# Optimization experiments

Measured on AMD Instinct MI355X. Metric: run time of the kernel, lower is better.

## Reference

```python
import jax, jax.numpy as jnp
import numpy as np
from jax import lax

B, T, D = 4, 2048, 2048
H, K, V = 16, 128, 128
CONV_K = 4
EPS_G = 1e-6
LN_EPS = 1e-5


def _dconv_causal(x, w, b):
    # x: (B,T,C); w: (C,1,Kk) depthwise. torch pads both sides Kk-1 then slices [:T],
    # which equals a causal left-pad of Kk-1.
    y = lax.conv_general_dilated(
        jnp.transpose(x, (0, 2, 1)), w, (1,),
        [(w.shape[-1] - 1, 0)],
        dimension_numbers=('NCH', 'OIH', 'NCH'),
        feature_group_count=w.shape[0])
    return jnp.transpose(y + b[None, :, None], (0, 2, 1))


def _kda_scan(q, k, v, g, beta, scale):
    # q,k: (B,H,T,K); v: (B,H,T,V); g: (B,H,T,K) log-decay (channel-wise); beta: (B,H,T)
    # Gated delta rule: S_t = Diag(exp(g_t)) S_{t-1} + beta_t k_t (v_t - k_t^T Diag(exp(g_t)) S_{t-1})
    S0 = jnp.zeros(q.shape[:2] + (q.shape[-1], v.shape[-1]), q.dtype)

    def step(S, inp):
        qt, kt, vt, gt, bt = inp
        S = S * jnp.exp(gt)[..., :, None]                     # per-key-channel decay
        err = vt - jnp.einsum('bhk,bhkv->bhv', kt, S)         # delta correction
        S = S + bt[..., None, None] * kt[..., None] * err[..., None, :]
        o = scale * jnp.einsum('bhk,bhkv->bhv', qt, S)
        return S, o

    xs = tuple(jnp.moveaxis(t_, 2, 0) for t_ in (q, k, v, g)) + (jnp.moveaxis(beta, 2, 0),)
    _, o = lax.scan(step, S0, xs)
    return jnp.moveaxis(o, 0, 2)                              # (B,H,T,V)


def setup_inputs() -> dict:
    key = jax.random.key(0)
    ks = jax.random.split(key, 16)
    s = 0.02
    return {
        'x':   jax.random.normal(ks[0], (B, T, D), jnp.float32),
        'Wq':  jax.random.normal(ks[1], (H * K, D), jnp.float32) * s,
        'Wk':  jax.random.normal(ks[2], (H * K, D), jnp.float32) * s,
        'Wv':  jax.random.normal(ks[3], (H * V, D), jnp.float32) * s,
        'Wa':  jax.random.normal(ks[4], (H * V, D), jnp.float32) * s,
        'ba':  jax.random.normal(ks[5], (H * V,), jnp.float32) * s,
        'Wb':  jax.random.normal(ks[6], (H, D), jnp.float32) * s,
        'bb':  jax.random.normal(ks[7], (H,), jnp.float32) * s,
        'Wg':  jax.random.normal(ks[8], (H * V, D), jnp.float32) * s,
        'Wo':  jax.random.normal(ks[9], (D, H * V), jnp.float32) * s,
        'cqw': jax.random.normal(ks[10], (H * K, 1, CONV_K), jnp.float32) * 0.2,
        'cqb': jnp.zeros((H * K,), jnp.float32),
        'ckw': jax.random.normal(ks[11], (H * K, 1, CONV_K), jnp.float32) * 0.2,
        'ckb': jnp.zeros((H * K,), jnp.float32),
        'cvw': jax.random.normal(ks[12], (H * V, 1, CONV_K), jnp.float32) * 0.2,
        'cvb': jnp.zeros((H * V,), jnp.float32),
        'ln_w': jnp.ones((V,), jnp.float32),
        'ln_b': jnp.zeros((V,), jnp.float32),
    }


def reference(x, Wq, Wk, Wv, Wa, ba, Wb, bb, Wg, Wo,
              cqw, cqb, ckw, ckb, cvw, cvb, ln_w, ln_b):
    b, t, _ = x.shape
    scale = K ** -0.5
    q = jax.nn.silu(_dconv_causal(x @ Wq.T, cqw, cqb))
    k = jax.nn.silu(_dconv_causal(x @ Wk.T, ckw, ckb))
    v = jax.nn.silu(_dconv_causal(x @ Wv.T, cvw, cvb))
    q = q.reshape(b, t, H, K).transpose(0, 2, 1, 3)           # (B,H,T,K)
    k = k.reshape(b, t, H, K).transpose(0, 2, 1, 3)
    v = v.reshape(b, t, H, V).transpose(0, 2, 1, 3)
    a = jax.nn.sigmoid(x @ Wa.T + ba).reshape(b, t, H, V).transpose(0, 2, 1, 3)
    g = jnp.log(jnp.maximum(a, EPS_G))                        # log-space channel gate
    beta = jax.nn.sigmoid(x @ Wb.T + bb).transpose(0, 2, 1)   # (B,H,T)
    o = _kda_scan(q, k, v, g, beta, scale).transpose(0, 2, 1, 3)  # (B,T,H,V)
    mu = o.mean(-1, keepdims=True)
    var = ((o - mu) ** 2).mean(-1, keepdims=True)
    o = (o - mu) * lax.rsqrt(var + LN_EPS) * ln_w + ln_b      # per-head LayerNorm
    gate = jax.nn.sigmoid(x @ Wg.T).reshape(b, t, H, V)
    return ((o * gate).reshape(b, t, H * V)) @ Wo.T
```

## Files before the change

kernel.cpp:

```cpp
#include <hip/hip_runtime.h>
#include <cstdint>
#include <cstddef>

#define B_ 4
#define T_ 2048
#define D_ 2048
#define H_ 16

typedef __bf16 bf16x8 __attribute__((ext_vector_type(8)));
typedef float  f32x4  __attribute__((ext_vector_type(4)));
typedef unsigned short u16;
typedef u16 u16x8 __attribute__((ext_vector_type(8)));

__device__ __forceinline__ u16 f2bf(float f) {
    union { float f; unsigned u; } v; v.f = f;
    unsigned r = v.u + 0x7FFFu + ((v.u >> 16) & 1u);
    return (u16)(r >> 16);
}
__device__ __forceinline__ float bf2f(u16 h) {
    union { unsigned u; float f; } v; v.u = ((unsigned)h) << 16;
    return v.f;
}
__device__ __forceinline__ float sigmoidf_(float x) {
    return 1.f / (1.f + __expf(-x));
}
__device__ __forceinline__ void async_load16(const void* g, void* l) {
    __builtin_amdgcn_global_load_lds(
        (const __attribute__((address_space(1))) void*)g,
        (__attribute__((address_space(3))) void*)l,
        16, 0, 0);
}

__device__ __forceinline__ float row_allreduce16(float x) {
    int v;
    v = __builtin_amdgcn_update_dpp(0, __builtin_bit_cast(int, x), 0xB1, 0xF, 0xF, true);
    x += __builtin_bit_cast(float, v);
    v = __builtin_amdgcn_update_dpp(0, __builtin_bit_cast(int, x), 0x4E, 0xF, 0xF, true);
    x += __builtin_bit_cast(float, v);
    v = __builtin_amdgcn_update_dpp(0, __builtin_bit_cast(int, x), 0x140, 0xF, 0xF, true);
    x += __builtin_bit_cast(float, v);
    v = __builtin_amdgcn_update_dpp(0, __builtin_bit_cast(int, x), 0x141, 0xF, 0xF, true);
    x += __builtin_bit_cast(float, v);
    return x;
}

__global__ void cvt_bf16_k(const float* __restrict__ s, u16* __restrict__ d, int n) {
    int i = blockIdx.x * 256 + threadIdx.x;
    if (i < n) d[i] = f2bf(s[i]);
}

__global__ void pad_wb_k(const float* __restrict__ Wb, u16* __restrict__ d) {
    int i = blockIdx.x * 256 + threadIdx.x;
    d[i] = (i < 32768) ? f2bf(Wb[i]) : (u16)0;
}

__device__ __forceinline__ void store_c(float* p, float v) { *p = v; }
__device__ __forceinline__ void store_c(u16* p, float v) { *p = f2bf(v); }

template <typename OutT, int PERM>
__global__ __launch_bounds__(256) void gemm_bt(const u16* __restrict__ A,
                                               const u16* __restrict__ Bm,
                                               OutT* __restrict__ C, int K, int ldc) {
    __shared__ __align__(16) u16 smA[128 * 64];
    __shared__ __align__(16) u16 smB[128 * 64];
    const int tid  = threadIdx.x;
    const int lane = tid & 63;
    const int w    = tid >> 6;
    const int wm   = (w >> 1) * 64;
    const int wn   = (w & 1) * 64;
    const int bm   = blockIdx.x, bn = blockIdx.y;

    f32x4 acc[4][4];
#pragma unroll
    for (int i = 0; i < 4; ++i)
#pragma unroll
        for (int j = 0; j < 4; ++j) acc[i][j] = (f32x4){0.f, 0.f, 0.f, 0.f};

    const int rr = tid >> 3;
    const int cc = (tid & 7) * 8;
    const u16* Ag = A + (size_t)(bm * 128) * K;
    const u16* Bg = Bm + (size_t)(bn * 128) * K;

    for (int k0 = 0; k0 < K; k0 += 64) {
#pragma unroll
        for (int it = 0; it < 4; ++it) {
            async_load16(Ag + (size_t)(it * 32 + rr) * K + (k0 + cc), &smA[(it * 256 + tid) * 8]);
            async_load16(Bg + (size_t)(it * 32 + rr) * K + (k0 + cc), &smB[(it * 256 + tid) * 8]);
        }
        __syncthreads();
#pragma unroll
        for (int kk = 0; kk < 64; kk += 32) {
            bf16x8 af[4], bfr[4];
            const int qoff = kk + ((lane >> 4) * 8);
#pragma unroll
            for (int mi = 0; mi < 4; ++mi)
                af[mi] = *(const bf16x8*)&smA[(wm + mi * 16 + (lane & 15)) * 64 + qoff];
#pragma unroll
            for (int ni = 0; ni < 4; ++ni)
                bfr[ni] = *(const bf16x8*)&smB[(wn + ni * 16 + (lane & 15)) * 64 + qoff];
#pragma unroll
            for (int mi = 0; mi < 4; ++mi)
#pragma unroll
                for (int ni = 0; ni < 4; ++ni)
                    acc[mi][ni] = __builtin_amdgcn_mfma_f32_16x16x32_bf16(af[mi], bfr[ni], acc[mi][ni], 0, 0, 0);
        }
        __syncthreads();
    }

#pragma unroll
    for (int mi = 0; mi < 4; ++mi) {
        const int row0 = bm * 128 + wm + mi * 16 + ((lane >> 4) * 4);
#pragma unroll
        for (int ni = 0; ni < 4; ++ni) {
            int colg = bn * 128 + wn + ni * 16 + (lane & 15);
            if (PERM) colg = (colg & ~127) | (((colg & 15) << 3) | ((colg >> 4) & 7));
#pragma unroll
            for (int rg = 0; rg < 4; ++rg)
                store_c(&C[(size_t)(row0 + rg) * ldc + colg], acc[mi][ni][rg]);
        }
    }
}

template <int TRANSPOSE>
__global__ void conv_silu_k(const u16* __restrict__ pre,
                            const float* __restrict__ w, const float* __restrict__ bias,
                            u16* __restrict__ outp) {
    int idx = blockIdx.x * 256 + threadIdx.x;
    int c = idx & 2047;
    int t = (idx >> 11) & (T_ - 1);
    int b = idx >> 22;
    const u16* base = pre + (size_t)(b * T_ + t) * 2048 + c;
    float acc = bias[c];
#pragma unroll
    for (int j = 0; j < 4; ++j) {
        int tt = t - 3 + j;
        if (tt >= 0) {
            float xv = bf2f(base[(ptrdiff_t)(j - 3) * 2048]);
            acc = fmaf(xv, w[c * 4 + j], acc);
        }
    }
    float y = acc * sigmoidf_(acc);
    int h = c >> 7, cl = c & 127;
    int p = TRANSPOSE ? ((cl & 15) * 8 + (cl >> 4)) : cl;
    outp[((size_t)(b * H_ + h) * T_ + t) * 128 + p] = f2bf(y);
}

#define TB 8
__global__ __launch_bounds__(256) void kda_scan_k(const u16* __restrict__ qg,
                                                  const u16* __restrict__ kg,
                                                  const u16* __restrict__ vg,
                                                  const u16* __restrict__ ag,
                                                  const u16* __restrict__ bpg,
                                                  const float* __restrict__ bav,
                                                  const float* __restrict__ bbv,
                                                  u16* __restrict__ og) {
    const int blk = blockIdx.x;
    const int bh  = blk >> 3;
    const int vch = blk & 7;
    const int tid = threadIdx.x;
    const int col = tid >> 4;
    const int sl  = tid & 15;
    const int b = bh >> 4, h = bh & 15;

    __shared__ __align__(16) u16   sq[2][TB][128];
    __shared__ __align__(16) u16   sk[2][TB][128];
    __shared__ __align__(16) float sdA[2][TB][64];
    __shared__ __align__(16) float sdB[2][TB][64];
    __shared__ float sv[2][TB][16];
    __shared__ float sb_[2][TB];

    const u16* qb  = qg + (size_t)bh * T_ * 128;
    const u16* kb  = kg + (size_t)bh * T_ * 128;
    const u16* vb  = vg + (size_t)bh * T_ * 128 + vch * 16;
    const u16* ab  = ag + (size_t)b * T_ * 2048 + h * 128;
    const u16* bpb = bpg + (size_t)b * T_ * 128 + h;
    u16* op = og + (size_t)b * T_ * 2048 + h * 128 + vch * 16 + col;

    const int ur = tid >> 5;
    const int c4 = (tid & 31) * 4;
    const int chb = c4 >> 3;
    const int jb  = c4 & 7;
    const float rba0 = bav[h * 128 + (jb + 0) * 16 + chb];
    const float rba1 = bav[h * 128 + (jb + 1) * 16 + chb];
    const float rba2 = bav[h * 128 + (jb + 2) * 16 + chb];
    const float rba3 = bav[h * 128 + (jb + 3) * 16 + chb];
    const float bbh = bbv[h];
    float* dst_d = (c4 & 4) ? &sdB[0][0][0] : &sdA[0][0][0];
    const int doff = ur * 64 + chb * 4;
    const int dstride = TB * 64;

    float S[8];
#pragma unroll
    for (int j = 0; j < 8; ++j) S[j] = 0.f;

    ushort4 rq, rk, ra;
    float rv = 0.f, rbet = 0.f;
    rq = *(const ushort4*)(qb + tid * 4);
    rk = *(const ushort4*)(kb + tid * 4);
    ra = *(const ushort4*)(ab + (size_t)ur * 2048 + c4);
    if (tid < 128) rv = bf2f(vb[(size_t)(tid >> 4) * 128 + (tid & 15)]);
    if (tid < TB) rbet = bf2f(bpb[(size_t)tid * 128]);

    const float scale = 0.08838834764831845f;
    const int NM = T_ / TB;
    for (int m = 0; m < NM; ++m) {
        const int pb = m & 1;
        float4 fd = {fmaxf(sigmoidf_(bf2f(ra.x) + rba0), 1e-6f),
                     fmaxf(sigmoidf_(bf2f(ra.y) + rba1), 1e-6f),
                     fmaxf(sigmoidf_(bf2f(ra.z) + rba2), 1e-6f),
                     fmaxf(sigmoidf_(bf2f(ra.w) + rba3), 1e-6f)};
        *(ushort4*)(&sq[pb][0][0] + tid * 4) = rq;
        *(ushort4*)(&sk[pb][0][0] + tid * 4) = rk;
        *(float4*)(dst_d + pb * dstride + doff) = fd;
        if (tid < 128) sv[pb][tid >> 4][tid & 15] = rv;
        if (tid < TB) sb_[pb][tid] = sigmoidf_(rbet + bbh);
        __syncthreads();
        if (m + 1 < NM) {
            size_t t0n = (size_t)(m + 1) * TB;
            rq = *(const ushort4*)(qb + t0n * 128 + tid * 4);
            rk = *(const ushort4*)(kb + t0n * 128 + tid * 4);
            ra = *(const ushort4*)(ab + (t0n + ur) * 2048 + c4);
            if (tid < 128) rv = bf2f(vb[(t0n + (tid >> 4)) * 128 + (tid & 15)]);
            if (tid < TB) rbet = bf2f(bpb[(t0n + tid) * 128]);
        }
#pragma unroll
        for (int u = 0; u < TB; ++u) {
            u16x8 q8 = *(const u16x8*)&sq[pb][u][sl * 8];
            u16x8 k8 = *(const u16x8*)&sk[pb][u][sl * 8];
            float4 dA = *(const float4*)&sdA[pb][u][sl * 4];
            float4 dB = *(const float4*)&sdB[pb][u][sl * 4];
            float kf[8], qf[8], dv[8];
#pragma unroll
            for (int j = 0; j < 8; ++j) { kf[j] = bf2f(k8[j]); qf[j] = bf2f(q8[j]); }
            dv[0] = dA.x; dv[1] = dA.y; dv[2] = dA.z; dv[3] = dA.w;
            dv[4] = dB.x; dv[5] = dB.y; dv[6] = dB.z; dv[7] = dB.w;
            float e0 = 0.f, e1 = 0.f;
#pragma unroll
            for (int j = 0; j < 8; j += 2) {
                S[j]     *= dv[j];     e0 = fmaf(kf[j],     S[j],     e0);
                S[j + 1] *= dv[j + 1]; e1 = fmaf(kf[j + 1], S[j + 1], e1);
            }
            float errp = row_allreduce16(e0 + e1);
            float uu = sb_[pb][u] * (sv[pb][u][col] - errp);
            float o0 = 0.f, o1 = 0.f;
#pragma unroll
            for (int j = 0; j < 8; j += 2) {
                S[j]     = fmaf(kf[j],     uu, S[j]);     o0 = fmaf(qf[j],     S[j],     o0);
                S[j + 1] = fmaf(kf[j + 1], uu, S[j + 1]); o1 = fmaf(qf[j + 1], S[j + 1], o1);
            }
            float outv = row_allreduce16(o0 + o1);
            if (sl == 0) op[(size_t)(m * TB + u) * 2048] = f2bf(scale * outv);
        }
        __syncthreads();
    }
}

__global__ __launch_bounds__(256) void ln_gate_k(const u16* __restrict__ o,
                                                 const u16* __restrict__ gpre,
                                                 const float* __restrict__ lnw,
                                                 const float* __restrict__ lnb,
                                                 u16* __restrict__ act) {
    int inst = blockIdx.x * 4 + (threadIdx.x >> 6);
    int lane = threadIdx.x & 63;
    int bt = inst >> 4, h = inst & 15;
    const u16* opr = o + (size_t)bt * 2048 + h * 128;
    ushort2 xr = *(const ushort2*)(opr + lane * 2);
    float x0 = bf2f(xr.x), x1 = bf2f(xr.y);
    float s  = x0 + x1;
    float ss = x0 * x0 + x1 * x1;
#pragma unroll
    for (int msk = 1; msk < 64; msk <<= 1) {
        s  += __shfl_xor(s, msk);
        ss += __shfl_xor(ss, msk);
    }
    float mu   = s * (1.f / 128.f);
    float var  = ss * (1.f / 128.f) - mu * mu;
    float rstd = rsqrtf(var + 1e-5f);
    const u16* gp = gpre + (size_t)bt * 2048 + h * 128 + lane * 2;
    u16* ap = act + (size_t)bt * 2048 + h * 128 + lane * 2;
#pragma unroll
    for (int e = 0; e < 2; ++e) {
        int v = lane * 2 + e;
        float xx = (e == 0) ? x0 : x1;
        float y = (xx - mu) * rstd * lnw[v] + lnb[v];
        float gate = sigmoidf_(bf2f(gp[e]));
        ap[e] = f2bf(y * gate);
    }
}

extern "C" void kernel_launch(void* const* d_in, const int* in_sizes, int n_in,
                              void* d_out, int out_size, void* d_ws, size_t ws_size,
                              hipStream_t stream) {
    (void)in_sizes; (void)n_in; (void)out_size; (void)ws_size;
    const float* x   = (const float*)d_in[0];
    const float* Wq  = (const float*)d_in[1];
    const float* Wk  = (const float*)d_in[2];
    const float* Wv  = (const float*)d_in[3];
    const float* Wa  = (const float*)d_in[4];
    const float* ba  = (const float*)d_in[5];
    const float* Wb  = (const float*)d_in[6];
    const float* bbv = (const float*)d_in[7];
    const float* Wg  = (const float*)d_in[8];
    const float* Wo  = (const float*)d_in[9];
    const float* cqw = (const float*)d_in[10];
    const float* cqb = (const float*)d_in[11];
    const float* ckw = (const float*)d_in[12];
    const float* ckb = (const float*)d_in[13];
    const float* cvw = (const float*)d_in[14];
    const float* cvb = (const float*)d_in[15];
    const float* lnw = (const float*)d_in[16];
    const float* lnb = (const float*)d_in[17];
    float* out = (float*)d_out;

    char* p = (char*)d_ws;
    size_t off = 0;
    auto take = [&](size_t bytes) -> char* {
        char* r = p + off;
        off += (bytes + 255) & ~(size_t)255;
        return r;
    };
    u16* Wslot = (u16*)take((size_t)4194304 * 2);
    u16* qpre  = (u16*)take((size_t)16777216 * 2);
    u16* kpre  = (u16*)take((size_t)16777216 * 2);
    u16* vpre  = (u16*)take((size_t)16777216 * 2);
    u16* apre  = (u16*)take((size_t)16777216 * 2);
    u16* bpre  = (u16*)take((size_t)1048576 * 2);

    u16* xb  = (u16*)d_out;
    u16* qsc = (u16*)d_out + 16777216;
    u16* ksc  = qpre;
    u16* vsc  = kpre;
    u16* ob   = vpre;
    u16* gpre = qpre;
    u16* act  = kpre;

    cvt_bf16_k<<<65536, 256, 0, stream>>>(x, xb, 16777216);

    cvt_bf16_k<<<16384, 256, 0, stream>>>(Wq, Wslot, 4194304);
    gemm_bt<u16, 0><<<dim3(64, 16), 256, 0, stream>>>(xb, Wslot, qpre, 2048, 2048);
    cvt_bf16_k<<<16384, 256, 0, stream>>>(Wk, Wslot, 4194304);
    gemm_bt<u16, 0><<<dim3(64, 16), 256, 0, stream>>>(xb, Wslot, kpre, 2048, 2048);
    cvt_bf16_k<<<16384, 256, 0, stream>>>(Wv, Wslot, 4194304);
    gemm_bt<u16, 0><<<dim3(64, 16), 256, 0, stream>>>(xb, Wslot, vpre, 2048, 2048);
    cvt_bf16_k<<<16384, 256, 0, stream>>>(Wa, Wslot, 4194304);
    gemm_bt<u16, 1><<<dim3(64, 16), 256, 0, stream>>>(xb, Wslot, apre, 2048, 2048);
    pad_wb_k<<<1024, 256, 0, stream>>>(Wb, Wslot);
    gemm_bt<u16, 0><<<dim3(64, 1), 256, 0, stream>>>(xb, Wslot, bpre, 2048, 128);

    conv_silu_k<1><<<65536, 256, 0, stream>>>(qpre, cqw, cqb, qsc);
    conv_silu_k<1><<<65536, 256, 0, stream>>>(kpre, ckw, ckb, ksc);
    conv_silu_k<0><<<65536, 256, 0, stream>>>(vpre, cvw, cvb, vsc);

    kda_scan_k<<<512, 256, 0, stream>>>(qsc, ksc, vsc, apre, bpre, ba, bbv, ob);

    cvt_bf16_k<<<16384, 256, 0, stream>>>(Wg, Wslot, 4194304);
    gemm_bt<u16, 0><<<dim3(64, 16), 256, 0, stream>>>(xb, Wslot, gpre, 2048, 2048);

    ln_gate_k<<<32768, 256, 0, stream>>>(ob, gpre, lnw, lnb, act);

    cvt_bf16_k<<<16384, 256, 0, stream>>>(Wo, Wslot, 4194304);
    gemm_bt<float, 0><<<dim3(64, 16), 256, 0, stream>>>(act, Wslot, out, 2048, 2048);
}
```

Before: 1.904 ms.

## Split scan state across 32 lanes per value column with 512-thread blocks

The KDA scan kernel now uses 512 threads per block. Each value column's 128-key state is spread over 32 lanes holding 4 entries each, instead of 16 lanes holding 8, which halves the serial per-step work per thread at the cost of an extra cross-half shuffle in each reduction. Q, K and the decay are converted to fp32 once when staged into shared memory. The step tile grows to 16 timesteps, and the block index is remapped to interleave batch-heads across blocks. The permuted channel layout in the GEMM epilogue and the conv kernel is changed to match the new 4-wide per-lane grouping.

Measured after the change: 1.800 ms. -5.5%, faster.

```diff
diff --git a/kernel.cpp b/kernel.cpp
--- a/kernel.cpp
+++ b/kernel.cpp
@@ -41,6 +41,12 @@
     x += __builtin_bit_cast(float, v);
     v = __builtin_amdgcn_update_dpp(0, __builtin_bit_cast(int, x), 0x141, 0xF, 0xF, true);
     x += __builtin_bit_cast(float, v);
+    return x;
+}
+
+__device__ __forceinline__ float grp32_allreduce(float x) {
+    x = row_allreduce16(x);
+    x += __shfl_xor(x, 32);
     return x;
 }
 
@@ -113,7 +119,10 @@
 #pragma unroll
         for (int ni = 0; ni < 4; ++ni) {
             int colg = bn * 128 + wn + ni * 16 + (lane & 15);
-            if (PERM) colg = (colg & ~127) | (((colg & 15) << 3) | ((colg >> 4) & 7));
+            if (PERM) {
+                int cl = colg & 127;
+                colg = (colg & ~127) | (((cl & 31) << 2) | (cl >> 5));
+            }
 #pragma unroll
             for (int rg = 0; rg < 4; ++rg)
                 store_c(&C[(size_t)(row0 + rg) * ldc + colg], acc[mi][ni][rg]);
@@ -141,115 +150,106 @@
     }
     float y = acc * sigmoidf_(acc);
     int h = c >> 7, cl = c & 127;
-    int p = TRANSPOSE ? ((cl & 15) * 8 + (cl >> 4)) : cl;
+    int p = TRANSPOSE ? (((cl & 31) << 2) | (cl >> 5)) : cl;
     outp[((size_t)(b * H_ + h) * T_ + t) * 128 + p] = f2bf(y);
 }
 
-#define TB 8
-__global__ __launch_bounds__(256) void kda_scan_k(const u16* __restrict__ qg,
-                                                  const u16* __restrict__ kg,
-                                                  const u16* __restrict__ vg,
-                                                  const u16* __restrict__ ag,
-                                                  const u16* __restrict__ bpg,
-                                                  const float* __restrict__ bav,
-                                                  const float* __restrict__ bbv,
-                                                  u16* __restrict__ og) {
+#define TB2 16
+__global__ __launch_bounds__(512, 4) void kda_scan_k(const u16* __restrict__ qg,
+                                                     const u16* __restrict__ kg,
+                                                     const u16* __restrict__ vg,
+                                                     const u16* __restrict__ ag,
+                                                     const u16* __restrict__ bpg,
+                                                     const float* __restrict__ bav,
+                                                     const float* __restrict__ bbv,
+                                                     u16* __restrict__ og) {
     const int blk = blockIdx.x;
-    const int bh  = blk >> 3;
-    const int vch = blk & 7;
+    const int bh  = (blk & 7) * 8 + (blk >> 6);
+    const int vch = (blk >> 3) & 7;
     const int tid = threadIdx.x;
-    const int col = tid >> 4;
-    const int sl  = tid & 15;
+    const int lane = tid & 63;
+    const int w    = tid >> 6;
+    const int colIdx = w * 2 + ((lane >> 4) & 1);
+    const int kidx   = (lane & 15) + ((lane >> 5) << 4);
     const int b = bh >> 4, h = bh & 15;
 
-    __shared__ __align__(16) u16   sq[2][TB][128];
-    __shared__ __align__(16) u16   sk[2][TB][128];
-    __shared__ __align__(16) float sdA[2][TB][64];
-    __shared__ __align__(16) float sdB[2][TB][64];
-    __shared__ float sv[2][TB][16];
-    __shared__ float sb_[2][TB];
+    __shared__ __align__(16) float sq[2][TB2][128];
+    __shared__ __align__(16) float sk[2][TB2][128];
+    __shared__ __align__(16) float sd[2][TB2][128];
+    __shared__ float sv[2][TB2][16];
+    __shared__ float sb_[2][TB2];
 
     const u16* qb  = qg + (size_t)bh * T_ * 128;
     const u16* kb  = kg + (size_t)bh * T_ * 128;
     const u16* vb  = vg + (size_t)bh * T_ * 128 + vch * 16;
     const u16* ab  = ag + (size_t)b * T_ * 2048 + h * 128;
     const u16* bpb = bpg + (size_t)b * T_ * 128 + h;
-    u16* op = og + (size_t)b * T_ * 2048 + h * 128 + vch * 16 + col;
+    u16* op = og + (size_t)b * T_ * 2048 + h * 128 + vch * 16 + colIdx;
 
     const int ur = tid >> 5;
-    const int c4 = (tid & 31) * 4;
-    const int chb = c4 >> 3;
-    const int jb  = c4 & 7;
-    const float rba0 = bav[h * 128 + (jb + 0) * 16 + chb];
-    const float rba1 = bav[h * 128 + (jb + 1) * 16 + chb];
-    const float rba2 = bav[h * 128 + (jb + 2) * 16 + chb];
-    const float rba3 = bav[h * 128 + (jb + 3) * 16 + chb];
+    const int p4 = (tid & 31) * 4;
+    const float rba0 = bav[h * 128 +  0 + (tid & 31)];
+    const float rba1 = bav[h * 128 + 32 + (tid & 31)];
+    const float rba2 = bav[h * 128 + 64 + (tid & 31)];
+    const float rba3 = bav[h * 128 + 96 + (tid & 31)];
     const float bbh = bbv[h];
-    float* dst_d = (c4 & 4) ? &sdB[0][0][0] : &sdA[0][0][0];
-    const int doff = ur * 64 + chb * 4;
-    const int dstride = TB * 64;
-
-    float S[8];
-#pragma unroll
-    for (int j = 0; j < 8; ++j) S[j] = 0.f;
+
+    float S[4];
+#pragma unroll
+    for (int j = 0; j < 4; ++j) S[j] = 0.f;
 
     ushort4 rq, rk, ra;
     float rv = 0.f, rbet = 0.f;
-    rq = *(const ushort4*)(qb + tid * 4);
-    rk = *(const ushort4*)(kb + tid * 4);
-    ra = *(const ushort4*)(ab + (size_t)ur * 2048 + c4);
-    if (tid < 128) rv = bf2f(vb[(size_t)(tid >> 4) * 128 + (tid & 15)]);
-    if (tid < TB) rbet = bf2f(bpb[(size_t)tid * 128]);
+    rq = *(const ushort4*)(qb + (size_t)ur * 128 + p4);
+    rk = *(const ushort4*)(kb + (size_t)ur * 128 + p4);
+    ra = *(const ushort4*)(ab + (size_t)ur * 2048 + p4);
+    if (tid < 256) rv = bf2f(vb[(size_t)(tid >> 4) * 128 + (tid & 15)]);
+    if (tid < TB2) rbet = bf2f(bpb[(size_t)tid * 128]);
 
     const float scale = 0.08838834764831845f;
-    const int NM = T_ / TB;
+    const int NM = T_ / TB2;
     for (int m = 0; m < NM; ++m) {
         const int pb = m & 1;
+        float4 fq = {bf2f(rq.x), bf2f(rq.y), bf2f(rq.z), bf2f(rq.w)};
+        float4 fk = {bf2f(rk.x), bf2f(rk.y), bf2f(rk.z), bf2f(rk.w)};
         float4 fd = {fmaxf(sigmoidf_(bf2f(ra.x) + rba0), 1e-6f),
                      fmaxf(sigmoidf_(bf2f(ra.y) + rba1), 1e-6f),
                      fmaxf(sigmoidf_(bf2f(ra.z) + rba2), 1e-6f),
                      fmaxf(sigmoidf_(bf2f(ra.w) + rba3), 1e-6f)};
-        *(ushort4*)(&sq[pb][0][0] + tid * 4) = rq;
-        *(ushort4*)(&sk[pb][0][0] + tid * 4) = rk;
-        *(float4*)(dst_d + pb * dstride + doff) = fd;
-        if (tid < 128) sv[pb][tid >> 4][tid & 15] = rv;
-        if (tid < TB) sb_[pb][tid] = sigmoidf_(rbet + bbh);
+        *(float4*)&sq[pb][ur][p4] = fq;
+        *(float4*)&sk[pb][ur][p4] = fk;
+        *(float4*)&sd[pb][ur][p4] = fd;
+        if (tid < 256) sv[pb][tid >> 4][tid & 15] = rv;
+        if (tid < TB2) sb_[pb][tid] = sigmoidf_(rbet + bbh);
         __syncthreads();
         if (m + 1 < NM) {
-            size_t t0n = (size_t)(m + 1) * TB;
-            rq = *(const ushort4*)(qb + t0n * 128 + tid * 4);
-            rk = *(const ushort4*)(kb + t0n * 128 + tid * 4);
-            ra = *(const ushort4*)(ab + (t0n + ur) * 2048 + c4);
-            if (tid < 128) rv = bf2f(vb[(t0n + (tid >> 4)) * 128 + (tid & 15)]);
-            if (tid < TB) rbet = bf2f(bpb[(t0n + tid) * 128]);
-        }
-#pragma unroll
-        for (int u = 0; u < TB; ++u) {
-            u16x8 q8 = *(const u16x8*)&sq[pb][u][sl * 8];
-            u16x8 k8 = *(const u16x8*)&sk[pb][u][sl * 8];
-            float4 dA = *(const float4*)&sdA[pb][u][sl * 4];
-            float4 dB = *(const float4*)&sdB[pb][u][sl * 4];
-            float kf[8], qf[8], dv[8];
-#pragma unroll
-            for (int j = 0; j < 8; ++j) { kf[j] = bf2f(k8[j]); qf[j] = bf2f(q8[j]); }
-            dv[0] = dA.x; dv[1] = dA.y; dv[2] = dA.z; dv[3] = dA.w;
-            dv[4] = dB.x; dv[5] = dB.y; dv[6] = dB.z; dv[7] = dB.w;
-            float e0 = 0.f, e1 = 0.f;
-#pragma unroll
-            for (int j = 0; j < 8; j += 2) {
-                S[j]     *= dv[j];     e0 = fmaf(kf[j],     S[j],     e0);
-                S[j + 1] *= dv[j + 1]; e1 = fmaf(kf[j + 1], S[j + 1], e1);
-            }
-            float errp = row_allreduce16(e0 + e1);
-            float uu = sb_[pb][u] * (sv[pb][u][col] - errp);
-            float o0 = 0.f, o1 = 0.f;
-#pragma unroll
-            for (int j = 0; j < 8; j += 2) {
-                S[j]     = fmaf(kf[j],     uu, S[j]);     o0 = fmaf(qf[j],     S[j],     o0);
-                S[j + 1] = fmaf(kf[j + 1], uu, S[j + 1]); o1 = fmaf(qf[j + 1], S[j + 1], o1);
-            }
-            float outv = row_allreduce16(o0 + o1);
-            if (sl == 0) op[(size_t)(m * TB + u) * 2048] = f2bf(scale * outv);
+            size_t t0n = (size_t)(m + 1) * TB2;
+            rq = *(const ushort4*)(qb + (t0n + ur) * 128 + p4);
+            rk = *(const ushort4*)(kb + (t0n + ur) * 128 + p4);
+            ra = *(const ushort4*)(ab + (t0n + ur) * 2048 + p4);
+            if (tid < 256) rv = bf2f(vb[(t0n + (tid >> 4)) * 128 + (tid & 15)]);
+            if (tid < TB2) rbet = bf2f(bpb[(t0n + tid) * 128]);
+        }
+#pragma unroll
+        for (int u = 0; u < TB2; ++u) {
+            float4 q4 = *(const float4*)&sq[pb][u][kidx * 4];
+            float4 k4 = *(const float4*)&sk[pb][u][kidx * 4];
+            float4 d4 = *(const float4*)&sd[pb][u][kidx * 4];
+            float e0, e1;
+            S[0] *= d4.x; e0 = k4.x * S[0];
+            S[1] *= d4.y; e1 = k4.y * S[1];
+            S[2] *= d4.z; e0 = fmaf(k4.z, S[2], e0);
+            S[3] *= d4.w; e1 = fmaf(k4.w, S[3], e1);
+            float errp = grp32_allreduce(e0 + e1);
+            float uu = sb_[pb][u] * (sv[pb][u][colIdx] - errp);
+            float o0, o1;
+            S[0] = fmaf(k4.x, uu, S[0]); o0 = q4.x * S[0];
+            S[1] = fmaf(k4.y, uu, S[1]); o1 = q4.y * S[1];
+            S[2] = fmaf(k4.z, uu, S[2]); o0 = fmaf(q4.z, S[2], o0);
+            S[3] = fmaf(k4.w, uu, S[3]); o1 = fmaf(q4.w, S[3], o1);
+            float outv = grp32_allreduce(o0 + o1);
+            if (((lane & 15) | (lane >> 5)) == 0)
+                op[(size_t)(m * TB2 + u) * 2048] = f2bf(scale * outv);
         }
         __syncthreads();
     }
@@ -351,7 +351,7 @@
     conv_silu_k<1><<<65536, 256, 0, stream>>>(kpre, ckw, ckb, ksc);
     conv_silu_k<0><<<65536, 256, 0, stream>>>(vpre, cvw, cvb, vsc);
 
-    kda_scan_k<<<512, 256, 0, stream>>>(qsc, ksc, vsc, apre, bpre, ba, bbv, ob);
+    kda_scan_k<<<512, 512, 0, stream>>>(qsc, ksc, vsc, apre, bpre, ba, bbv, ob);
 
     cvt_bf16_k<<<16384, 256, 0, stream>>>(Wg, Wslot, 4194304);
     gemm_bt<u16, 0><<<dim3(64, 16), 256, 0, stream>>>(xb, Wslot, gpre, 2048, 2048);
```

## Restructure scan to 512-thread blocks with 32 value columns, XCD-aware mapping, vectorize conversion

Applied to the files above, without the earlier changes.

The scan kernel now runs 256 blocks of 512 threads, each covering 32 value columns and 16 timesteps per staging step instead of 16 columns and 8 timesteps. Block indices are remapped so that blocks sharing a (batch, head) land on the same XCD. The goal is to halve redundant q/k/decay loads across blocks and halve the number of barriers per sequence, at the cost of fewer blocks in flight. The fp32-to-bf16 conversion kernel is also vectorized to process four elements per thread, with correspondingly smaller grids.

New measurement: 1.694 ms. 1.12x faster.

```diff
diff --git a/kernel.cpp b/kernel.cpp
--- a/kernel.cpp
+++ b/kernel.cpp
@@ -46,7 +46,11 @@
 
 __global__ void cvt_bf16_k(const float* __restrict__ s, u16* __restrict__ d, int n) {
     int i = blockIdx.x * 256 + threadIdx.x;
-    if (i < n) d[i] = f2bf(s[i]);
+    if (i * 4 < n) {
+        float4 v = *(const float4*)(s + (size_t)i * 4);
+        ushort4 o = {f2bf(v.x), f2bf(v.y), f2bf(v.z), f2bf(v.w)};
+        *(ushort4*)(d + (size_t)i * 4) = o;
+    }
 }
 
 __global__ void pad_wb_k(const float* __restrict__ Wb, u16* __restrict__ d) {
@@ -145,36 +149,40 @@
     outp[((size_t)(b * H_ + h) * T_ + t) * 128 + p] = f2bf(y);
 }
 
-#define TB 8
-__global__ __launch_bounds__(256) void kda_scan_k(const u16* __restrict__ qg,
-                                                  const u16* __restrict__ kg,
-                                                  const u16* __restrict__ vg,
-                                                  const u16* __restrict__ ag,
-                                                  const u16* __restrict__ bpg,
-                                                  const float* __restrict__ bav,
-                                                  const float* __restrict__ bbv,
-                                                  u16* __restrict__ og) {
+#define TB2 16
+__global__ __launch_bounds__(512, 2) void kda_scan_k(const u16* __restrict__ qg,
+                                                     const u16* __restrict__ kg,
+                                                     const u16* __restrict__ vg,
+                                                     const u16* __restrict__ ag,
+                                                     const u16* __restrict__ bpg,
+                                                     const float* __restrict__ bav,
+                                                     const float* __restrict__ bbv,
+                                                     u16* __restrict__ og) {
     const int blk = blockIdx.x;
-    const int bh  = blk >> 3;
-    const int vch = blk & 7;
+    const int xcd = blk & 7;
+    const int ci  = (blk >> 3) & 7;
+    const int vch = blk >> 6;
+    const int bh  = xcd * 8 + ci;
     const int tid = threadIdx.x;
-    const int col = tid >> 4;
-    const int sl  = tid & 15;
+    const int lane = tid & 63;
+    const int w    = tid >> 6;
+    const int colIdx = w * 4 + (lane >> 4);
+    const int sl     = lane & 15;
     const int b = bh >> 4, h = bh & 15;
 
-    __shared__ __align__(16) u16   sq[2][TB][128];
-    __shared__ __align__(16) u16   sk[2][TB][128];
-    __shared__ __align__(16) float sdA[2][TB][64];
-    __shared__ __align__(16) float sdB[2][TB][64];
-    __shared__ float sv[2][TB][16];
-    __shared__ float sb_[2][TB];
+    __shared__ __align__(16) u16   sq[2][TB2][128];
+    __shared__ __align__(16) u16   sk[2][TB2][128];
+    __shared__ __align__(16) float sdA[2][TB2][64];
+    __shared__ __align__(16) float sdB[2][TB2][64];
+    __shared__ float sv[2][TB2][32];
+    __shared__ float sb_[2][TB2];
 
     const u16* qb  = qg + (size_t)bh * T_ * 128;
     const u16* kb  = kg + (size_t)bh * T_ * 128;
-    const u16* vb  = vg + (size_t)bh * T_ * 128 + vch * 16;
+    const u16* vst = vg + (size_t)bh * T_ * 128 + vch * 32 + (tid & 31);
     const u16* ab  = ag + (size_t)b * T_ * 2048 + h * 128;
     const u16* bpb = bpg + (size_t)b * T_ * 128 + h;
-    u16* op = og + (size_t)b * T_ * 2048 + h * 128 + vch * 16 + col;
+    u16* op = og + (size_t)b * T_ * 2048 + h * 128 + vch * 32 + colIdx;
 
     const int ur = tid >> 5;
     const int c4 = (tid & 31) * 4;
@@ -187,49 +195,49 @@
     const float bbh = bbv[h];
     float* dst_d = (c4 & 4) ? &sdB[0][0][0] : &sdA[0][0][0];
     const int doff = ur * 64 + chb * 4;
-    const int dstride = TB * 64;
+    const int dstride = TB2 * 64;
 
     float S[8];
 #pragma unroll
     for (int j = 0; j < 8; ++j) S[j] = 0.f;
 
-    ushort4 rq, rk, ra;
-    float rv = 0.f, rbet = 0.f;
-    rq = *(const ushort4*)(qb + tid * 4);
-    rk = *(const ushort4*)(kb + tid * 4);
-    ra = *(const ushort4*)(ab + (size_t)ur * 2048 + c4);
-    if (tid < 128) rv = bf2f(vb[(size_t)(tid >> 4) * 128 + (tid & 15)]);
-    if (tid < TB) rbet = bf2f(bpb[(size_t)tid * 128]);
+    ushort4 rq = *(const ushort4*)(qb + (size_t)ur * 128 + c4);
+    ushort4 rk = *(const ushort4*)(kb + (size_t)ur * 128 + c4);
+    ushort4 ra = *(const ushort4*)(ab + (size_t)ur * 2048 + c4);
+    u16 rv = vst[(size_t)ur * 128];
+    float rbet = (tid < TB2) ? bf2f(bpb[(size_t)tid * 128]) : 0.f;
 
     const float scale = 0.08838834764831845f;
-    const int NM = T_ / TB;
+    const int NM = T_ / TB2;
     for (int m = 0; m < NM; ++m) {
         const int pb = m & 1;
         float4 fd = {fmaxf(sigmoidf_(bf2f(ra.x) + rba0), 1e-6f),
                      fmaxf(sigmoidf_(bf2f(ra.y) + rba1), 1e-6f),
                      fmaxf(sigmoidf_(bf2f(ra.z) + rba2), 1e-6f),
                      fmaxf(sigmoidf_(bf2f(ra.w) + rba3), 1e-6f)};
-        *(ushort4*)(&sq[pb][0][0] + tid * 4) = rq;
-        *(ushort4*)(&sk[pb][0][0] + tid * 4) = rk;
+        *(ushort4*)&sq[pb][ur][c4] = rq;
+        *(ushort4*)&sk[pb][ur][c4] = rk;
         *(float4*)(dst_d + pb * dstride + doff) = fd;
-        if (tid < 128) sv[pb][tid >> 4][tid & 15] = rv;
-        if (tid < TB) sb_[pb][tid] = sigmoidf_(rbet + bbh);
+        sv[pb][ur][tid & 31] = bf2f(rv);
+        if (tid < TB2) sb_[pb][tid] = sigmoidf_(rbet + bbh);
         __syncthreads();
         if (m + 1 < NM) {
-            size_t t0n = (size_t)(m + 1) * TB;
-            rq = *(const ushort4*)(qb + t0n * 128 + tid * 4);
-            rk = *(const ushort4*)(kb + t0n * 128 + tid * 4);
+            size_t t0n = (size_t)(m + 1) * TB2;
+            rq = *(const ushort4*)(qb + (t0n + ur) * 128 + c4);
+            rk = *(const ushort4*)(kb + (t0n + ur) * 128 + c4);
             ra = *(const ushort4*)(ab + (t0n + ur) * 2048 + c4);
-            if (tid < 128) rv = bf2f(vb[(t0n + (tid >> 4)) * 128 + (tid & 15)]);
-            if (tid < TB) rbet = bf2f(bpb[(t0n + tid) * 128]);
-        }
-#pragma unroll
-        for (int u = 0; u < TB; ++u) {
+            rv = vst[(t0n + ur) * 128];
+            if (tid < TB2) rbet = bf2f(bpb[(t0n + tid) * 128]);
+        }
+#pragma unroll
+        for (int u = 0; u < TB2; ++u) {
             u16x8 q8 = *(const u16x8*)&sq[pb][u][sl * 8];
             u16x8 k8 = *(const u16x8*)&sk[pb][u][sl * 8];
             float4 dA = *(const float4*)&sdA[pb][u][sl * 4];
             float4 dB = *(const float4*)&sdB[pb][u][sl * 4];
-            float kf[8], qf[8], dv[8];
+            float fv  = sv[pb][u][colIdx];
+            float sbv = sb_[pb][u];
+            float qf[8], kf[8], dv[8];
 #pragma unroll
             for (int j = 0; j < 8; ++j) { kf[j] = bf2f(k8[j]); qf[j] = bf2f(q8[j]); }
             dv[0] = dA.x; dv[1] = dA.y; dv[2] = dA.z; dv[3] = dA.w;
@@ -241,7 +249,7 @@
                 S[j + 1] *= dv[j + 1]; e1 = fmaf(kf[j + 1], S[j + 1], e1);
             }
             float errp = row_allreduce16(e0 + e1);
-            float uu = sb_[pb][u] * (sv[pb][u][col] - errp);
+            float uu = sbv * (fv - errp);
             float o0 = 0.f, o1 = 0.f;
 #pragma unroll
             for (int j = 0; j < 8; j += 2) {
@@ -249,7 +257,8 @@
                 S[j + 1] = fmaf(kf[j + 1], uu, S[j + 1]); o1 = fmaf(qf[j + 1], S[j + 1], o1);
             }
             float outv = row_allreduce16(o0 + o1);
-            if (sl == 0) op[(size_t)(m * TB + u) * 2048] = f2bf(scale * outv);
+            if (sl == 0)
+                op[(size_t)(m * TB2 + u) * 2048] = f2bf(scale * outv);
         }
         __syncthreads();
     }
@@ -334,15 +343,15 @@
     u16* gpre = qpre;
     u16* act  = kpre;
 
-    cvt_bf16_k<<<65536, 256, 0, stream>>>(x, xb, 16777216);
-
-    cvt_bf16_k<<<16384, 256, 0, stream>>>(Wq, Wslot, 4194304);
+    cvt_bf16_k<<<16384, 256, 0, stream>>>(x, xb, 16777216);
+
+    cvt_bf16_k<<<4096, 256, 0, stream>>>(Wq, Wslot, 4194304);
     gemm_bt<u16, 0><<<dim3(64, 16), 256, 0, stream>>>(xb, Wslot, qpre, 2048, 2048);
-    cvt_bf16_k<<<16384, 256, 0, stream>>>(Wk, Wslot, 4194304);
+    cvt_bf16_k<<<4096, 256, 0, stream>>>(Wk, Wslot, 4194304);
     gemm_bt<u16, 0><<<dim3(64, 16), 256, 0, stream>>>(xb, Wslot, kpre, 2048, 2048);
-    cvt_bf16_k<<<16384, 256, 0, stream>>>(Wv, Wslot, 4194304);
+    cvt_bf16_k<<<4096, 256, 0, stream>>>(Wv, Wslot, 4194304);
     gemm_bt<u16, 0><<<dim3(64, 16), 256, 0, stream>>>(xb, Wslot, vpre, 2048, 2048);
-    cvt_bf16_k<<<16384, 256, 0, stream>>>(Wa, Wslot, 4194304);
+    cvt_bf16_k<<<4096, 256, 0, stream>>>(Wa, Wslot, 4194304);
     gemm_bt<u16, 1><<<dim3(64, 16), 256, 0, stream>>>(xb, Wslot, apre, 2048, 2048);
     pad_wb_k<<<1024, 256, 0, stream>>>(Wb, Wslot);
     gemm_bt<u16, 0><<<dim3(64, 1), 256, 0, stream>>>(xb, Wslot, bpre, 2048, 128);
@@ -351,13 +360,13 @@
     conv_silu_k<1><<<65536, 256, 0, stream>>>(kpre, ckw, ckb, ksc);
     conv_silu_k<0><<<65536, 256, 0, stream>>>(vpre, cvw, cvb, vsc);
 
-    kda_scan_k<<<512, 256, 0, stream>>>(qsc, ksc, vsc, apre, bpre, ba, bbv, ob);
-
-    cvt_bf16_k<<<16384, 256, 0, stream>>>(Wg, Wslot, 4194304);
+    kda_scan_k<<<256, 512, 0, stream>>>(qsc, ksc, vsc, apre, bpre, ba, bbv, ob);
+
+    cvt_bf16_k<<<4096, 256, 0, stream>>>(Wg, Wslot, 4194304);
     gemm_bt<u16, 0><<<dim3(64, 16), 256, 0, stream>>>(xb, Wslot, gpre, 2048, 2048);
 
     ln_gate_k<<<32768, 256, 0, stream>>>(ob, gpre, lnw, lnb, act);
 
-    cvt_bf16_k<<<16384, 256, 0, stream>>>(Wo, Wslot, 4194304);
+    cvt_bf16_k<<<4096, 256, 0, stream>>>(Wo, Wslot, 4194304);
     gemm_bt<float, 0><<<dim3(64, 16), 256, 0, stream>>>(act, Wslot, out, 2048, 2048);
 }
```
